# Performance work log

Hardware: AMD Instinct MI355X
Metric: run time of the kernel (lower is better)

Reference implementation:

```python
import jax, jax.numpy as jnp
import numpy as np
from jax import lax

L, B, N, D = 6, 4, 2048, 512
H, DH = 8, 64
ID = H * DH           # 512
M = 266               # int(64*log(64)) random features
INNER = 2 * D         # conformer expansion
K = 31                # depthwise kernel
PAD = (15, 15)        # calc_same_padding(31)
EPS_LN = 1e-5


def setup_inputs() -> dict:
    key = jax.random.key(0)
    ks = jax.random.split(key, 12)
    s = 0.02
    return {
        "x": jax.random.normal(ks[0], (B, N, D), jnp.float32),
        "ln1_g": jnp.ones((L, D), jnp.float32),
        "ln1_b": jnp.zeros((L, D), jnp.float32),
        "wq": jax.random.normal(ks[1], (L, ID, D), jnp.float32) * s,
        "bq": jnp.zeros((L, ID), jnp.float32),
        "wk": jax.random.normal(ks[2], (L, ID, D), jnp.float32) * s,
        "bk": jnp.zeros((L, ID), jnp.float32),
        "wv": jax.random.normal(ks[3], (L, ID, D), jnp.float32) * s,
        "bv": jnp.zeros((L, ID), jnp.float32),
        "wo": jax.random.normal(ks[4], (L, ID, D), jnp.float32) * s,
        "bo": jnp.zeros((L, D), jnp.float32),
        # FAVOR+ random projection buffer (gaussian orthogonal ~ iid gaussian rows)
        "proj": jax.random.normal(ks[5], (L, M, DH), jnp.float32),
        "ln2_g": jnp.ones((L, D), jnp.float32),
        "ln2_b": jnp.zeros((L, D), jnp.float32),
        "pw1_w": jax.random.normal(ks[6], (L, 2 * INNER, D), jnp.float32) * s,
        "pw1_b": jnp.zeros((L, 2 * INNER), jnp.float32),
        "dw_w": jax.random.normal(ks[7], (L, INNER, K), jnp.float32) * s,
        "dw_b": jnp.zeros((L, INNER), jnp.float32),
        "pw2_w": jax.random.normal(ks[8], (L, D, INNER), jnp.float32) * s,
        "pw2_b": jnp.zeros((L, D), jnp.float32),
    }


def layer_norm(x, g, b):
    mu = jnp.mean(x, axis=-1, keepdims=True)
    var = jnp.mean((x - mu) ** 2, axis=-1, keepdims=True)
    return (x - mu) * lax.rsqrt(var + EPS_LN) * g + b


def softmax_kernel(data, proj, is_query, eps=1e-4):
    # data: [b,h,n,dh], proj: [m,dh]
    dn = DH ** -0.25
    ratio = M ** -0.5
    data_dash = jnp.einsum('bhnd,md->bhnm', dn * data, proj)
    diag = jnp.sum(data * data, axis=-1, keepdims=True) * 0.5 * dn * dn  # [b,h,n,1]
    if is_query:
        mx = jnp.max(data_dash, axis=-1, keepdims=True)
        return ratio * (jnp.exp(data_dash - diag - mx) + eps)
    else:
        return ratio * jnp.exp(data_dash - diag + eps)


def favor_attention(q, k, v, proj):
    qp = softmax_kernel(q, proj, True)   # [b,h,n,m]
    kp = softmax_kernel(k, proj, False)  # [b,h,n,m]
    k_cumsum = jnp.sum(kp, axis=-2)      # [b,h,m]
    d_inv = 1.0 / (jnp.einsum('bhnm,bhm->bhn', qp, k_cumsum) + 1e-8)
    context = jnp.einsum('bhnm,bhne->bhme', kp, v)          # [b,h,m,dh]
    out = jnp.einsum('bhme,bhnm,bhn->bhne', context, qp, d_inv)
    return out


def pcmer_forward(x, ln1_g, ln1_b, wq, bq, wk, bk, wv, bv, wo, bo, proj,
                  ln2_g, ln2_b, pw1_w, pw1_b, dw_w, dw_b, pw2_w, pw2_b):
    for l in range(L):
        # --- self attention (FAVOR+) ---
        h = layer_norm(x, ln1_g[l], ln1_b[l])
        q = (h @ wq[l].T + bq[l]).reshape(B, N, H, DH).transpose(0, 2, 1, 3)
        k = (h @ wk[l].T + bk[l]).reshape(B, N, H, DH).transpose(0, 2, 1, 3)
        v = (h @ wv[l].T + bv[l]).reshape(B, N, H, DH).transpose(0, 2, 1, 3)
        o = favor_attention(q, k, v, proj[l])                 # [b,h,n,dh]
        o = o.transpose(0, 2, 1, 3).reshape(B, N, ID)
        x = x + (o @ wo[l].T + bo[l])
        # --- conformer conv module ---
        h = layer_norm(x, ln2_g[l], ln2_b[l])
        y = h @ pw1_w[l].T + pw1_b[l]                         # [b,n,2*inner]
        a, g = y[..., :INNER], y[..., INNER:]
        y = a * jax.nn.sigmoid(g)                             # GLU
        yt = jnp.pad(y.transpose(0, 2, 1), ((0, 0), (0, 0), PAD))  # [b,inner,n+30]
        dw = lax.conv_general_dilated(
            yt, dw_w[l][:, None, :], window_strides=(1,), padding='VALID',
            feature_group_count=INNER,
            dimension_numbers=('NCH', 'OIH', 'NCH')) + dw_b[l][None, :, None]
        dw = jax.nn.silu(dw).transpose(0, 2, 1)               # [b,n,inner]
        x = x + (dw @ pw2_w[l].T + pw2_b[l])
    return x


def reference(x, ln1_g, ln1_b, wq, bq, wk, bk, wv, bv, wo, bo, proj,
              ln2_g, ln2_b, pw1_w, pw1_b, dw_w, dw_b, pw2_w, pw2_b):
    return pcmer_forward(x, ln1_g, ln1_b, wq, bq, wk, bk, wv, bv, wo, bo, proj,
                         ln2_g, ln2_b, pw1_w, pw1_b, dw_w, dw_b, pw2_w, pw2_b)
```

## Files before the change

### kernel.cpp

```cpp
#include <hip/hip_runtime.h>


#define L_LAYERS 6
#define B_ 4
#define N_ 2048
#define D_ 512
#define H_ 8
#define DH_ 64
#define M_ 266
#define INNER_ 1024
#define T_ 8192
#define PS_ 320
#define QKVS_ 1536
#define NS_ 8

typedef __attribute__((ext_vector_type(8))) short short8;
typedef __attribute__((ext_vector_type(4))) float floatx4;

__device__ __forceinline__ ushort f2bf(float f) {
  union { float f; uint u; } v; v.f = f;
  uint r = v.u + 0x7fffu + ((v.u >> 16) & 1u);
  return (ushort)(r >> 16);
}
__device__ __forceinline__ float bf2f(ushort u) {
  union { uint u; float f; } v; v.u = ((uint)u) << 16;
  return v.f;
}
__device__ __forceinline__ float wave_sum(float v) {
#pragma unroll
  for (int m = 1; m < 64; m <<= 1) v += __shfl_xor(v, m);
  return v;
}
__device__ __forceinline__ void async_cp16(const void* g, void* l) {
  __builtin_amdgcn_global_load_lds(
      (const __attribute__((address_space(1))) void*)g,
      (__attribute__((address_space(3))) void*)l, 16, 0, 0);
}

__global__ void f2bf4_kernel(const float4* __restrict__ in, ushort* __restrict__ out, int n4) {
  int i = blockIdx.x * 256 + threadIdx.x;
  if (i < n4) {
    float4 v = in[i];
    ushort4 r;
    r.x = f2bf(v.x); r.y = f2bf(v.y); r.z = f2bf(v.z); r.w = f2bf(v.w);
    *(ushort4*)(out + (size_t)i * 4) = r;
  }
}
__global__ void pack_qkv_w(const float4* __restrict__ src, ushort* __restrict__ dst, int off) {
  int i = blockIdx.x * 256 + threadIdx.x;
  if (i >= L_LAYERS * 512 * 128) return;
  int l = i >> 16;
  int rem = i & 65535;
  int row = rem >> 7, c4 = rem & 127;
  float4 v = src[i];
  ushort4 r;
  r.x = f2bf(v.x); r.y = f2bf(v.y); r.z = f2bf(v.z); r.w = f2bf(v.w);
  *(ushort4*)(dst + ((size_t)l * QKVS_ + off + row) * 512 + c4 * 4) = r;
}
__global__ void pack_qkv_b(const float* __restrict__ bq, const float* __restrict__ bk,
                           const float* __restrict__ bv, float* __restrict__ dst) {
  int i = blockIdx.x * 256 + threadIdx.x;
  if (i >= L_LAYERS * QKVS_) return;
  int l = i / QKVS_, c = i % QKVS_;
  dst[i] = c < 512 ? bq[l * 512 + c] : (c < 1024 ? bk[l * 512 + c - 512] : bv[l * 512 + c - 1024]);
}
__global__ void pad_proj(const float* __restrict__ proj, ushort* __restrict__ dst) {
  int i = blockIdx.x * 256 + threadIdx.x;
  if (i >= L_LAYERS * 320 * 64) return;
  int l = i / (320 * 64), rem = i % (320 * 64), m = rem >> 6, kk = rem & 63;
  dst[i] = (m < M_) ? f2bf(proj[((size_t)l * M_ + m) * 64 + kk]) : (ushort)0;
}
__global__ void pack_pw1_w(const float4* __restrict__ src, ushort* __restrict__ dst) {
  int i = blockIdx.x * 256 + threadIdx.x;
  if (i >= L_LAYERS * 2048 * 128) return;
  int l = i >> 18;
  int rem = i & 262143;
  int cp = rem >> 7, c4 = rem & 127;
  int s = (cp >> 4) & 1;
  int srow = ((cp >> 5) << 4) + (cp & 15) + s * 1024;
  float4 v = src[((size_t)l * 2048 + srow) * 128 + c4];
  ushort4 r;
  r.x = f2bf(v.x); r.y = f2bf(v.y); r.z = f2bf(v.z); r.w = f2bf(v.w);
  *(ushort4*)(dst + ((size_t)l * 2048 + cp) * 512 + c4 * 4) = r;
}
__global__ void pack_pw1_b(const float* __restrict__ src, float* __restrict__ dst) {
  int i = blockIdx.x * 256 + threadIdx.x;
  if (i >= L_LAYERS * 2048) return;
  int l = i >> 11, cp = i & 2047;
  int s = (cp >> 4) & 1;
  int srow = ((cp >> 5) << 4) + (cp & 15) + s * 1024;
  dst[i] = src[l * 2048 + srow];
}

__global__ __launch_bounds__(256) void ln_kernel(const float* __restrict__ x,
                                                 const float* __restrict__ g,
                                                 const float* __restrict__ b,
                                                 ushort* __restrict__ out) {
  const int t = blockIdx.x;
  const int tid = threadIdx.x;
  const float* row = x + (size_t)t * D_;
  float v0 = row[tid], v1 = row[tid + 256];
  float s1 = v0 + v1;
  float s2 = v0 * v0 + v1 * v1;
  s1 = wave_sum(s1);
  s2 = wave_sum(s2);
  __shared__ float sh1[4], sh2[4];
  int w = tid >> 6;
  if ((tid & 63) == 0) { sh1[w] = s1; sh2[w] = s2; }
  __syncthreads();
  s1 = sh1[0] + sh1[1] + sh1[2] + sh1[3];
  s2 = sh2[0] + sh2[1] + sh2[2] + sh2[3];
  float mu = s1 * (1.f / D_);
  float var = s2 * (1.f / D_) - mu * mu;
  float rs = rsqrtf(var + 1e-5f);
  out[(size_t)t * D_ + tid]       = f2bf((v0 - mu) * rs * g[tid] + b[tid]);
  out[(size_t)t * D_ + tid + 256] = f2bf((v1 - mu) * rs * g[tid + 256] + b[tid + 256]);
}

template <bool HAS_RES, bool OUT_BF16, int ACT, int KT>
__global__ __launch_bounds__(256) void gemm_mfma(const ushort* __restrict__ A,
                                                 const ushort* __restrict__ W,
                                                 const float* __restrict__ bias,
                                                 const float* __restrict__ res,
                                                 void* __restrict__ Cout,
                                                 int ldc) {
  constexpr int NT = KT / 32;
  __shared__ ushort As[3][128 * 32];
  __shared__ ushort Bs[3][128 * 32];
  const int tid = threadIdx.x;
  const int w = tid >> 6, lane = tid & 63;
  const int row0 = blockIdx.x * 128, col0 = blockIdx.y * 128;
  const int rl = lane >> 2;
  const int lc = ((lane & 3) ^ ((lane >> 3) & 3)) * 8;
  const ushort* gA0 = A + (size_t)(row0 + w * 32 + rl) * KT + lc;
  const ushort* gA1 = gA0 + (size_t)16 * KT;
  const ushort* gB0 = W + (size_t)(col0 + w * 32 + rl) * KT + lc;
  const ushort* gB1 = gB0 + (size_t)16 * KT;
  const int m16 = lane & 15, quad = lane >> 4;
  const int awr = (w >> 1) * 64, bwc = (w & 1) * 64;
  floatx4 acc[4][4] = {};

  auto stage = [&](int t, int buf) {
    async_cp16(gA0 + t * 32, As[buf] + w * 1024);
    async_cp16(gA1 + t * 32, As[buf] + w * 1024 + 512);
    async_cp16(gB0 + t * 32, Bs[buf] + w * 1024);
    async_cp16(gB1 + t * 32, Bs[buf] + w * 1024 + 512);
  };
  auto body = [&](int buf, bool bar2) {
    short8 af[4], bfr[4];
#pragma unroll
    for (int i = 0; i < 4; i++) {
      int r = awr + i * 16 + m16;
      af[i] = *(const short8*)&As[buf][r * 32 + (quad ^ ((r >> 1) & 3)) * 8];
    }
#pragma unroll
    for (int j = 0; j < 4; j++) {
      int r = bwc + j * 16 + m16;
      bfr[j] = *(const short8*)&Bs[buf][r * 32 + (quad ^ ((r >> 1) & 3)) * 8];
    }
    if (bar2) {
      asm volatile("s_waitcnt lgkmcnt(0)" ::: "memory");
      __builtin_amdgcn_sched_barrier(0);
      __builtin_amdgcn_s_barrier();
    }
#pragma unroll
    for (int i = 0; i < 4; i++)
#pragma unroll
      for (int j = 0; j < 4; j++)
        acc[i][j] = __builtin_amdgcn_mfma_f32_16x16x32_bf16(af[i], bfr[j], acc[i][j], 0, 0, 0);
  };

  stage(0, 0);
  stage(1, 1);
  int c = 0;
  for (int t = 0; t < NT - 2; t++) {
    int pf = c + 2; if (pf >= 3) pf -= 3;
    stage(t + 2, pf);
    asm volatile("s_waitcnt vmcnt(8)" ::: "memory");
    __builtin_amdgcn_s_barrier();
    body(c, true);
    c++; if (c >= 3) c -= 3;
  }
  asm volatile("s_waitcnt vmcnt(4)" ::: "memory");
  __builtin_amdgcn_s_barrier();
  body(c, false);
  c++; if (c >= 3) c -= 3;
  asm volatile("s_waitcnt vmcnt(0)" ::: "memory");
  __builtin_amdgcn_s_barrier();
  body(c, false);

  if (ACT == 0) {
#pragma unroll
    for (int i = 0; i < 4; i++) {
      const int r0 = row0 + awr + i * 16 + quad * 4;
#pragma unroll
      for (int j = 0; j < 4; j++) {
        const int cc = col0 + bwc + j * 16 + m16;
        const float bv = bias[cc];
#pragma unroll
        for (int r = 0; r < 4; r++) {
          float vv = acc[i][j][r] + bv;
          if (HAS_RES) vv += res[(size_t)(r0 + r) * ldc + cc];
          if (OUT_BF16) ((ushort*)Cout)[(size_t)(r0 + r) * ldc + cc] = f2bf(vv);
          else          ((float*)Cout)[(size_t)(r0 + r) * ldc + cc] = vv;
        }
      }
    }
  } else {
#pragma unroll
    for (int i = 0; i < 4; i++) {
      const int r0 = row0 + awr + i * 16 + quad * 4;
#pragma unroll
      for (int jp = 0; jp < 2; jp++) {
        const int j = jp * 2;
        const int ca = col0 + bwc + j * 16 + m16;
        const float ba = bias[ca], bg = bias[ca + 16];
        const int oc = ((col0 + bwc) >> 1) + jp * 16 + m16;
#pragma unroll
        for (int r = 0; r < 4; r++) {
          float a = acc[i][j][r] + ba;
          float g = acc[i][j + 1][r] + bg;
          float z = a / (1.f + expf(-g));
          ((ushort*)Cout)[(size_t)(r0 + r) * ldc + oc] = f2bf(z);
        }
      }
    }
  }
}

__global__ __launch_bounds__(256) void ctx_phi_mfma(const ushort* __restrict__ qkv,
                                                    const ushort* __restrict__ projp,
                                                    float* __restrict__ part,
                                                    float* __restrict__ kpart) {
  __shared__ ushort projs[64 * 64];
  __shared__ ushort kts[32 * 64];
  __shared__ ushort kps[64][40];
  __shared__ ushort vsT[64][40];
  __shared__ float diag_sh[32];
  __shared__ float kshare[4][64];
  const int bh = blockIdx.x, mt = blockIdx.y, ns = blockIdx.z;
  const int b = bh >> 3, h = bh & 7;
  const int m0 = mt * 64;
  const int tid = threadIdx.x;
  const int w = tid >> 6, lane = tid & 63, l16 = lane & 15, quad = lane >> 4;
  const int rl8 = lane >> 3;
  const int lc8 = ((lane & 7) ^ (rl8 & 7)) * 8;
#pragma unroll
  for (int j = 0; j < 2; j++) {
    const int rb = w * 16 + j * 8;
    async_cp16(projp + (size_t)(m0 + rb + rl8) * 64 + lc8, projs + rb * 64);
  }
  const int nn = tid >> 3;
  const int a8 = tid & 7;
  const int gn = nn >> 3, jn = nn & 7;
  const int pc = ((gn ^ (a8 & 3)) << 3) | jn;
  const int km = tid & 63, kg = tid >> 6;
  const float dn = 0.35355339059327373f;
  const float ratio = 0.06131393394849658f;
  floatx4 acc[4] = {};
  float ksp = 0.f;
  for (int nstep = 0; nstep < 2048 / NS_ / 32; nstep++) {
    const int n0 = ns * (2048 / NS_) + nstep * 32;
    {
      const int rb = w * 8;
      async_cp16(qkv + (size_t)(b * N_ + n0 + rb + rl8) * QKVS_ + 512 + h * 64 + lc8,
                 kts + rb * 64);
    }
    uint4 vv = *(const uint4*)(qkv + ((size_t)(b * N_ + n0 + nn)) * QKVS_ + 1024 + h * 64 + a8 * 8);
    __syncthreads();
    {
      const int r = tid >> 3;
      const int c = tid & 7;
      short8 kv8 = *(const short8*)&kts[r * 64 + c * 8];
      const ushort* u = (const ushort*)&kv8;
      float s = 0.f;
#pragma unroll
      for (int j = 0; j < 8; j++) { float f = bf2f(u[j]); s += f * f; }
      s += __shfl_xor(s, 1);
      s += __shfl_xor(s, 2);
      s += __shfl_xor(s, 4);
      if ((tid & 7) == 0) diag_sh[r] = 0.0625f * s;
    }
    {
      const ushort* ve = (const ushort*)&vv;
#pragma unroll
      for (int j = 0; j < 8; j++) vsT[a8 * 8 + j][pc] = ve[j];
    }
    __syncthreads();
    floatx4 pacc[2] = {};
#pragma unroll
    for (int s = 0; s < 2; s++) {
      const int ar = w * 16 + l16;
      short8 af = *(const short8*)&projs[ar * 64 + ((s * 4 + quad) ^ (ar & 7)) * 8];
#pragma unroll
      for (int nj = 0; nj < 2; nj++) {
        const int br = nj * 16 + l16;
        short8 bf = *(const short8*)&kts[br * 64 + ((s * 4 + quad) ^ (br & 7)) * 8];
        pacc[nj] = __builtin_amdgcn_mfma_f32_16x16x32_bf16(af, bf, pacc[nj], 0, 0, 0);
      }
    }
#pragma unroll
    for (int nj = 0; nj < 2; nj++) {
      const int n = nj * 16 + l16;
      const float dgn = diag_sh[n];
#pragma unroll
      for (int r = 0; r < 4; r++) {
        const int m = w * 16 + quad * 4 + r;
        float val = (m0 + m < M_) ? ratio * expf(dn * pacc[nj][r] - dgn + 1e-4f) : 0.f;
        kps[m][(((n >> 3) ^ ((m >> 3) & 3)) << 3) | (n & 7)] = f2bf(val);
      }
    }
    __syncthreads();
    const int am = w * 16 + l16;
    const int apg = quad ^ ((am >> 3) & 3);
    short8 af = *(const short8*)&kps[am][apg * 8];
#pragma unroll
    for (int et = 0; et < 4; et++) {
      const int be = et * 16 + l16;
      const int bpg = quad ^ ((be >> 3) & 3);
      short8 bf = *(const short8*)&vsT[be][bpg * 8];
      acc[et] = __builtin_amdgcn_mfma_f32_16x16x32_bf16(af, bf, acc[et], 0, 0, 0);
    }
    {
      short8 kr = *(const short8*)&kps[km][kg * 8];
      const ushort* ku = (const ushort*)&kr;
#pragma unroll
      for (int j = 0; j < 8; j++) ksp += bf2f(ku[j]);
    }
  }
  float* pb = part + ((size_t)(bh * NS_ + ns) * 5 + mt) * 4096;
#pragma unroll
  for (int et = 0; et < 4; et++)
#pragma unroll
    for (int r = 0; r < 4; r++)
      pb[(w * 16 + quad * 4 + r) * 64 + et * 16 + l16] = acc[et][r];
  kshare[kg][km] = ksp;
  __syncthreads();
  if (tid < 64)
    kpart[((size_t)(bh * NS_ + ns) * 5 + mt) * 64 + tid] =
        kshare[0][tid] + kshare[1][tid] + kshare[2][tid] + kshare[3][tid];
}

__global__ __launch_bounds__(256) void ctx_reduce(const float* __restrict__ part,
                                                  const float* __restrict__ kpart,
                                                  ushort* __restrict__ ctxbT,
                                                  float* __restrict__ ksum) {
  const int bh = blockIdx.x, mt = blockIdx.y;
  const int tid = threadIdx.x;
  const int w = tid >> 6, lane = tid & 63;
  for (int oc = w; oc < 8; oc += 4) {
    const int mbase = mt * 64 + oc * 8;
    if (mbase < 288) {
      float s[8] = {0.f, 0.f, 0.f, 0.f, 0.f, 0.f, 0.f, 0.f};
#pragma unroll
      for (int ns = 0; ns < NS_; ns++) {
        const float* pb = part + ((size_t)(bh * NS_ + ns) * 5 + mt) * 4096;
#pragma unroll
        for (int ml = 0; ml < 8; ml++) s[ml] += pb[(oc * 8 + ml) * 64 + lane];
      }
      ushort tmp[8];
#pragma unroll
      for (int ml = 0; ml < 8; ml++) tmp[ml] = f2bf(s[ml]);
      *(short8*)(ctxbT + ((size_t)(bh * 64 + lane)) * 288 + mbase) = *(const short8*)tmp;
    }
  }
  if (tid < 64) {
    float s = 0.f;
#pragma unroll
    for (int ns = 0; ns < NS_; ns++)
      s += kpart[((size_t)(bh * NS_ + ns) * 5 + mt) * 64 + tid];
    ksum[(size_t)bh * PS_ + mt * 64 + tid] = s;
  }
}

__global__ __launch_bounds__(256, 4) void attn_fused(const ushort* __restrict__ qkv,
                                                     const ushort* __restrict__ projp,
                                                     const ushort* __restrict__ ctxbT,
                                                     const float* __restrict__ ksum,
                                                     ushort* __restrict__ o) {
  __shared__ __align__(16) ushort sm[14336];
  __shared__ float ks_sh[288];
  __shared__ float diag_sh[64];
  ushort* As = sm;
  ushort* Bs = sm + 4096;
  ushort (*qst)[40] = (ushort(*)[40])sm;
  const int bh = blockIdx.x, b = bh >> 3, h = bh & 7;
  const int n0 = blockIdx.y * 64;
  const int tid = threadIdx.x;
  const int w = tid >> 6, lane = tid & 63, l16 = lane & 15, quad = lane >> 4;
  const int rl8 = lane >> 3;
  const int lc8 = ((lane & 7) ^ (rl8 & 7)) * 8;
#pragma unroll
  for (int j = 0; j < 2; j++) {
    const int rb = w * 16 + j * 8;
    async_cp16(qkv + (size_t)(b * N_ + n0 + rb + rl8) * QKVS_ + h * 64 + lc8, As + rb * 64);
  }
#pragma unroll
  for (int j = 0; j < 5; j++) {
    const int rb = w * 40 + j * 8;
    async_cp16(projp + (size_t)(rb + rl8) * 64 + lc8, Bs + rb * 64);
  }
  for (int i = tid; i < 288; i += 256) ks_sh[i] = ksum[(size_t)bh * PS_ + i];
  __syncthreads();
  {
    const int r = w * 16 + (lane >> 2);
    const int c0 = 2 * (lane & 3);
    float s = 0.f;
#pragma unroll
    for (int cc = 0; cc < 2; cc++) {
      short8 vv = *(const short8*)&As[r * 64 + ((c0 + cc) ^ (r & 7)) * 8];
      const ushort* u = (const ushort*)&vv;
#pragma unroll
      for (int j = 0; j < 8; j++) { float f = bf2f(u[j]); s += f * f; }
    }
    s += __shfl_xor(s, 1);
    s += __shfl_xor(s, 2);
    if ((lane & 3) == 0) diag_sh[r] = 0.0625f * s;
  }
  __syncthreads();
  float dgr[4];
#pragma unroll
  for (int r = 0; r < 4; r++) dgr[r] = diag_sh[w * 16 + quad * 4 + r];
  floatx4 acc[18];
#pragma unroll
  for (int cf = 0; cf < 18; cf++) acc[cf] = (floatx4){0.f, 0.f, 0.f, 0.f};
  const int ar = w * 16 + l16;
#pragma unroll
  for (int s = 0; s < 2; s++) {
    short8 af = *(const short8*)&As[ar * 64 + ((s * 4 + quad) ^ (ar & 7)) * 8];
#pragma unroll
    for (int cf = 0; cf < 10; cf++) {
      const int br = cf * 16 + l16;
      short8 bf = *(const short8*)&Bs[br * 64 + ((s * 4 + quad) ^ (br & 7)) * 8];
      acc[cf] = __builtin_amdgcn_mfma_f32_16x16x32_bf16(af, bf, acc[cf], 0, 0, 0);
    }
  }
  __syncthreads();
#pragma unroll
  for (int j = 0; j < 4; j++) {
    const int rb = w * 32 + j * 8;
    async_cp16(projp + (size_t)(160 + rb + rl8) * 64 + lc8, Bs + rb * 64);
  }
  __syncthreads();
#pragma unroll
  for (int s = 0; s < 2; s++) {
    short8 af = *(const short8*)&As[ar * 64 + ((s * 4 + quad) ^ (ar & 7)) * 8];
#pragma unroll
    for (int cf = 10; cf < 18; cf++) {
      const int br = (cf - 10) * 16 + l16;
      short8 bf = *(const short8*)&Bs[br * 64 + ((s * 4 + quad) ^ (br & 7)) * 8];
      acc[cf] = __builtin_amdgcn_mfma_f32_16x16x32_bf16(af, bf, acc[cf], 0, 0, 0);
    }
  }
  const float dn = 0.35355339059327373f;
  const float ratio = 0.06131393394849658f;
  float mxr[4];
#pragma unroll
  for (int r = 0; r < 4; r++) {
    float mx = -1e30f;
#pragma unroll
    for (int cf = 0; cf < 18; cf++) {
      const int col = cf * 16 + l16;
      if (col < M_) mx = fmaxf(mx, dn * acc[cf][r]);
    }
    mx = fmaxf(mx, __shfl_xor(mx, 1));
    mx = fmaxf(mx, __shfl_xor(mx, 2));
    mx = fmaxf(mx, __shfl_xor(mx, 4));
    mx = fmaxf(mx, __shfl_xor(mx, 8));
    mxr[r] = mx;
  }
  __syncthreads();
  float dacc[4] = {0.f, 0.f, 0.f, 0.f};
  floatx4 acc2[4] = {};
  const ushort* ctxrow = ctxbT + (size_t)bh * (64 * 288);
  for (int m0 = 0; m0 < 288; m0 += 32) {
    const int cf0 = m0 >> 4;
#pragma unroll
    for (int cc = 0; cc < 2; cc++) {
      const int col = m0 + cc * 16 + l16;
      const float kv = ks_sh[col];
#pragma unroll
      for (int r = 0; r < 4; r++) {
        float val = (col < M_) ? ratio * (expf(dn * acc[cf0 + cc][r] - dgr[r] - mxr[r]) + 1e-4f)
                               : 0.f;
        qst[w * 16 + quad * 4 + r][cc * 16 + l16] = f2bf(val);
        dacc[r] += val * kv;
      }
    }
    short8 af = *(const short8*)&qst[w * 16 + l16][quad * 8];
#pragma unroll
    for (int et = 0; et < 4; et++) {
      short8 bf = *(const short8*)(ctxrow + (size_t)(et * 16 + l16) * 288 + m0 + quad * 8);
      acc2[et] = __builtin_amdgcn_mfma_f32_16x16x32_bf16(af, bf, acc2[et], 0, 0, 0);
    }
  }
  float di[4];
#pragma unroll
  for (int r = 0; r < 4; r++) {
    float d = dacc[r];
    d += __shfl_xor(d, 1);
    d += __shfl_xor(d, 2);
    d += __shfl_xor(d, 4);
    d += __shfl_xor(d, 8);
    di[r] = 1.f / (d + 1e-8f);
  }
#pragma unroll
  for (int r = 0; r < 4; r++) {
    const int n = n0 + w * 16 + quad * 4 + r;
#pragma unroll
    for (int et = 0; et < 4; et++)
      o[((size_t)(b * N_ + n)) * 512 + h * 64 + et * 16 + l16] = f2bf(acc2[et][r] * di[r]);
  }
}

#define TN_ 16
__global__ __launch_bounds__(256) void dwconv_kernel(const ushort* __restrict__ x,
                                                     const float* __restrict__ w,
                                                     const float* __restrict__ bias,
                                                     ushort* __restrict__ out) {
  const int bid = blockIdx.x;
  const int cb = bid & 3;
  const int nb = (bid >> 2) & 127;
  const int b  = bid >> 9;
  const int c = cb * 256 + threadIdx.x;
  const int n0 = nb * TN_;
  float win[TN_ + 30];
#pragma unroll
  for (int i = 0; i < TN_ + 30; i++) {
    int nn = n0 + i - 15;
    win[i] = (nn >= 0 && nn < N_) ? bf2f(x[(size_t)(b * N_ + nn) * INNER_ + c]) : 0.f;
  }
  float wc[31];
#pragma unroll
  for (int kk = 0; kk < 31; kk++) wc[kk] = w[c * 31 + kk];
  const float bsv = bias[c];
#pragma unroll
  for (int j = 0; j < TN_; j++) {
    float acc = bsv;
#pragma unroll
    for (int kk = 0; kk < 31; kk++) acc += win[j + kk] * wc[kk];
    acc = acc / (1.f + expf(-acc));
    out[(size_t)(b * N_ + n0 + j) * INNER_ + c] = f2bf(acc);
  }
}

extern "C" void kernel_launch(void* const* d_in, const int* in_sizes, int n_in,
                              void* d_out, int out_size, void* d_ws, size_t ws_size,
                              hipStream_t stream) {
  const float* in_x  = (const float*)d_in[0];
  const float* ln1_g = (const float*)d_in[1];
  const float* ln1_b = (const float*)d_in[2];
  const float* wq    = (const float*)d_in[3];
  const float* bq    = (const float*)d_in[4];
  const float* wk    = (const float*)d_in[5];
  const float* bk    = (const float*)d_in[6];
  const float* wv    = (const float*)d_in[7];
  const float* bv    = (const float*)d_in[8];
  const float* wo    = (const float*)d_in[9];
  const float* bo    = (const float*)d_in[10];
  const float* proj  = (const float*)d_in[11];
  const float* ln2_g = (const float*)d_in[12];
  const float* ln2_b = (const float*)d_in[13];
  const float* pw1_w = (const float*)d_in[14];
  const float* pw1_b = (const float*)d_in[15];
  const float* dw_w  = (const float*)d_in[16];
  const float* dw_b  = (const float*)d_in[17];
  const float* pw2_w = (const float*)d_in[18];
  const float* pw2_b = (const float*)d_in[19];

  char* cur = (char*)d_ws;
  auto alloc = [&](size_t bytes) { char* p = cur; cur += (bytes + 255) & ~(size_t)255; return p; };
  float*  x    = (float*)alloc((size_t)T_ * D_ * 4);
  ushort* p    = (ushort*)alloc((size_t)T_ * INNER_ * 2 * 2);
  float*  part = (float*)alloc((size_t)32 * NS_ * 5 * 4096 * 4);
  float*  kpart= (float*)alloc((size_t)32 * NS_ * 5 * 64 * 4);
  ushort* ctxb = (ushort*)alloc((size_t)32 * 288 * 64 * 2);
  float*  ksum = (float*)alloc((size_t)32 * PS_ * 4);
  ushort* h    = (ushort*)alloc((size_t)T_ * D_ * 2);
  ushort* qkv  = (ushort*)alloc((size_t)T_ * QKVS_ * 2);
  ushort* obuf = (ushort*)alloc((size_t)T_ * D_ * 2);
  ushort* wqkv_b = (ushort*)alloc((size_t)L_LAYERS * QKVS_ * 512 * 2);
  float*  bqkv   = (float*)alloc((size_t)L_LAYERS * QKVS_ * 4);
  ushort* wo_b = (ushort*)alloc((size_t)L_LAYERS * D_ * D_ * 2);
  ushort* pjp  = (ushort*)alloc((size_t)L_LAYERS * 320 * 64 * 2);
  ushort* p1_b = (ushort*)alloc((size_t)L_LAYERS * 2048 * D_ * 2);
  float*  pb1  = (float*)alloc((size_t)L_LAYERS * 2048 * 4);
  ushort* p2_b = (ushort*)alloc((size_t)L_LAYERS * D_ * INNER_ * 2);
  ushort* glu  = p;
  ushort* conv = p + (size_t)T_ * INNER_;

  pack_qkv_w<<<(L_LAYERS * 512 * 128 + 255) / 256, 256, 0, stream>>>((const float4*)wq, wqkv_b, 0);
  pack_qkv_w<<<(L_LAYERS * 512 * 128 + 255) / 256, 256, 0, stream>>>((const float4*)wk, wqkv_b, 512);
  pack_qkv_w<<<(L_LAYERS * 512 * 128 + 255) / 256, 256, 0, stream>>>((const float4*)wv, wqkv_b, 1024);
  pack_qkv_b<<<(L_LAYERS * QKVS_ + 255) / 256, 256, 0, stream>>>(bq, bk, bv, bqkv);
  pad_proj<<<(L_LAYERS * 320 * 64 + 255) / 256, 256, 0, stream>>>(proj, pjp);
  pack_pw1_w<<<(L_LAYERS * 2048 * 128 + 255) / 256, 256, 0, stream>>>((const float4*)pw1_w, p1_b);
  pack_pw1_b<<<(L_LAYERS * 2048 + 255) / 256, 256, 0, stream>>>(pw1_b, pb1);
  {
    int n4 = L_LAYERS * D_ * D_ / 4;
    f2bf4_kernel<<<(n4 + 255) / 256, 256, 0, stream>>>((const float4*)wo, wo_b, n4);
    n4 = L_LAYERS * D_ * INNER_ / 4;
    f2bf4_kernel<<<(n4 + 255) / 256, 256, 0, stream>>>((const float4*)pw2_w, p2_b, n4);
  }

  for (int l = 0; l < L_LAYERS; l++) {
    const ushort* wqkvl = wqkv_b + (size_t)l * QKVS_ * 512;
    const ushort* wol = wo_b + (size_t)l * D_ * D_;
    const ushort* pjl = pjp + (size_t)l * 320 * 64;
    const ushort* p1l = p1_b + (size_t)l * 2048 * D_;
    const ushort* p2l = p2_b + (size_t)l * D_ * INNER_;
    const float*  dwl = dw_w + (size_t)l * INNER_ * 31;
    const float*  dwbl = dw_b + (size_t)l * INNER_;
    const float*  xin = (l == 0) ? in_x : x;
    float* xout = (l == L_LAYERS - 1) ? (float*)d_out : x;

    ln_kernel<<<T_, 256, 0, stream>>>(xin, ln1_g + l * D_, ln1_b + l * D_, h);
    gemm_mfma<false, true, 0, 512><<<dim3(T_ / 128, QKVS_ / 128), 256, 0, stream>>>(
        h, wqkvl, bqkv + (size_t)l * QKVS_, nullptr, qkv, QKVS_);
    ctx_phi_mfma<<<dim3(32, 5, NS_), 256, 0, stream>>>(qkv, pjl, part, kpart);
    ctx_reduce<<<dim3(32, 5), 256, 0, stream>>>(part, kpart, ctxb, ksum);
    attn_fused<<<dim3(32, 32), 256, 0, stream>>>(qkv, pjl, ctxb, ksum, obuf);
    gemm_mfma<true, false, 0, 512><<<dim3(T_ / 128, 4), 256, 0, stream>>>(
        obuf, wol, bo + l * D_, xin, x, D_);
    ln_kernel<<<T_, 256, 0, stream>>>(x, ln2_g + l * D_, ln2_b + l * D_, h);
    gemm_mfma<false, true, 1, 512><<<dim3(T_ / 128, 16), 256, 0, stream>>>(
        h, p1l, pb1 + (size_t)l * 2048, nullptr, glu, INNER_);
    dwconv_kernel<<<B_ * (N_ / TN_) * 4, 256, 0, stream>>>(glu, dwl, dwbl, conv);
    gemm_mfma<true, false, 0, 1024><<<dim3(T_ / 128, 4), 256, 0, stream>>>(
        conv, p2l, pw2_b + l * D_, x, xout, D_);
  }
}
```

Before: 1.227 ms.

## Merge weight-packing launches, tune GEMM buffering, and streamline attention and conv kernels

Combines several one-time weight and bias packing kernels into fewer launches. Adds a buffer-count template parameter so the pw1 GEMM uses double instead of triple buffering, which lowers LDS use. In the attention kernel, Q is now loaded straight into registers with a shuffle-based diag reduction, MFMA sections get raised scheduling priority, the max uses a tree reduction, and output goes through LDS for wide coalesced stores. The depthwise conv doubles its tile length, and expf becomes __expf in several places, trading a little accuracy for cheaper math.

```diff
diff --git a/kernel.cpp b/kernel.cpp
--- a/kernel.cpp
+++ b/kernel.cpp
@@ -37,38 +37,55 @@
       (__attribute__((address_space(3))) void*)l, 16, 0, 0);
 }
 
-__global__ void f2bf4_kernel(const float4* __restrict__ in, ushort* __restrict__ out, int n4) {
+__global__ void f2bf4_dual(const float4* __restrict__ s1, int n1,
+                           const float4* __restrict__ s2, int n2,
+                           ushort* __restrict__ out) {
   int i = blockIdx.x * 256 + threadIdx.x;
-  if (i < n4) {
-    float4 v = in[i];
-    ushort4 r;
-    r.x = f2bf(v.x); r.y = f2bf(v.y); r.z = f2bf(v.z); r.w = f2bf(v.w);
-    *(ushort4*)(out + (size_t)i * 4) = r;
-  }
-}
-__global__ void pack_qkv_w(const float4* __restrict__ src, ushort* __restrict__ dst, int off) {
-  int i = blockIdx.x * 256 + threadIdx.x;
-  if (i >= L_LAYERS * 512 * 128) return;
-  int l = i >> 16;
-  int rem = i & 65535;
-  int row = rem >> 7, c4 = rem & 127;
-  float4 v = src[i];
+  if (i >= n1 + n2) return;
+  float4 v = (i < n1) ? s1[i] : s2[i - n1];
   ushort4 r;
   r.x = f2bf(v.x); r.y = f2bf(v.y); r.z = f2bf(v.z); r.w = f2bf(v.w);
-  *(ushort4*)(dst + ((size_t)l * QKVS_ + off + row) * 512 + c4 * 4) = r;
-}
-__global__ void pack_qkv_b(const float* __restrict__ bq, const float* __restrict__ bk,
-                           const float* __restrict__ bv, float* __restrict__ dst) {
+  *(ushort4*)(out + (size_t)i * 4) = r;
+}
+__global__ void pack_qkv_w3(const float4* __restrict__ wq, const float4* __restrict__ wk,
+                            const float4* __restrict__ wv, ushort* __restrict__ dst) {
   int i = blockIdx.x * 256 + threadIdx.x;
-  if (i >= L_LAYERS * QKVS_) return;
-  int l = i / QKVS_, c = i % QKVS_;
-  dst[i] = c < 512 ? bq[l * 512 + c] : (c < 1024 ? bk[l * 512 + c - 512] : bv[l * 512 + c - 1024]);
-}
-__global__ void pad_proj(const float* __restrict__ proj, ushort* __restrict__ dst) {
+  const int per = L_LAYERS * 512 * 128;
+  if (i >= 3 * per) return;
+  int seg = i / per;
+  int rem = i - seg * per;
+  const float4* src = seg == 0 ? wq : (seg == 1 ? wk : wv);
+  int l = rem >> 16;
+  int r2 = rem & 65535;
+  int row = r2 >> 7, c4 = r2 & 127;
+  float4 v = src[rem];
+  ushort4 r;
+  r.x = f2bf(v.x); r.y = f2bf(v.y); r.z = f2bf(v.z); r.w = f2bf(v.w);
+  *(ushort4*)(dst + ((size_t)l * QKVS_ + seg * 512 + row) * 512 + c4 * 4) = r;
+}
+__global__ void pack_small(const float* __restrict__ bq, const float* __restrict__ bk,
+                           const float* __restrict__ bv, float* __restrict__ bqkv,
+                           const float* __restrict__ proj, ushort* __restrict__ pjp,
+                           const float* __restrict__ pw1b, float* __restrict__ pb1) {
   int i = blockIdx.x * 256 + threadIdx.x;
-  if (i >= L_LAYERS * 320 * 64) return;
-  int l = i / (320 * 64), rem = i % (320 * 64), m = rem >> 6, kk = rem & 63;
-  dst[i] = (m < M_) ? f2bf(proj[((size_t)l * M_ + m) * 64 + kk]) : (ushort)0;
+  const int A = L_LAYERS * QKVS_;
+  const int Bn = L_LAYERS * 320 * 64;
+  const int C = L_LAYERS * 2048;
+  if (i < A) {
+    int l = i / QKVS_, c = i % QKVS_;
+    bqkv[i] = c < 512 ? bq[l * 512 + c]
+                      : (c < 1024 ? bk[l * 512 + c - 512] : bv[l * 512 + c - 1024]);
+  } else if (i < A + Bn) {
+    int j = i - A;
+    int l = j / (320 * 64), rem = j % (320 * 64), m = rem >> 6, kk = rem & 63;
+    pjp[j] = (m < M_) ? f2bf(proj[((size_t)l * M_ + m) * 64 + kk]) : (ushort)0;
+  } else if (i < A + Bn + C) {
+    int j = i - A - Bn;
+    int l = j >> 11, cp = j & 2047;
+    int s = (cp >> 4) & 1;
+    int srow = ((cp >> 5) << 4) + (cp & 15) + s * 1024;
+    pb1[j] = pw1b[l * 2048 + srow];
+  }
 }
 __global__ void pack_pw1_w(const float4* __restrict__ src, ushort* __restrict__ dst) {
   int i = blockIdx.x * 256 + threadIdx.x;
@@ -82,14 +99,6 @@
   ushort4 r;
   r.x = f2bf(v.x); r.y = f2bf(v.y); r.z = f2bf(v.z); r.w = f2bf(v.w);
   *(ushort4*)(dst + ((size_t)l * 2048 + cp) * 512 + c4 * 4) = r;
-}
-__global__ void pack_pw1_b(const float* __restrict__ src, float* __restrict__ dst) {
-  int i = blockIdx.x * 256 + threadIdx.x;
-  if (i >= L_LAYERS * 2048) return;
-  int l = i >> 11, cp = i & 2047;
-  int s = (cp >> 4) & 1;
-  int srow = ((cp >> 5) << 4) + (cp & 15) + s * 1024;
-  dst[i] = src[l * 2048 + srow];
 }
 
 __global__ __launch_bounds__(256) void ln_kernel(const float* __restrict__ x,
@@ -117,7 +126,7 @@
   out[(size_t)t * D_ + tid + 256] = f2bf((v1 - mu) * rs * g[tid + 256] + b[tid + 256]);
 }
 
-template <bool HAS_RES, bool OUT_BF16, int ACT, int KT>
+template <bool HAS_RES, bool OUT_BF16, int ACT, int KT, int BUFS>
 __global__ __launch_bounds__(256) void gemm_mfma(const ushort* __restrict__ A,
                                                  const ushort* __restrict__ W,
                                                  const float* __restrict__ bias,
@@ -125,8 +134,8 @@
                                                  void* __restrict__ Cout,
                                                  int ldc) {
   constexpr int NT = KT / 32;
-  __shared__ ushort As[3][128 * 32];
-  __shared__ ushort Bs[3][128 * 32];
+  __shared__ ushort As[BUFS][128 * 32];
+  __shared__ ushort Bs[BUFS][128 * 32];
   const int tid = threadIdx.x;
   const int w = tid >> 6, lane = tid & 63;
   const int row0 = blockIdx.x * 128, col0 = blockIdx.y * 128;
@@ -171,20 +180,23 @@
   };
 
   stage(0, 0);
-  stage(1, 1);
+  if (BUFS == 3) stage(1, 1);
   int c = 0;
-  for (int t = 0; t < NT - 2; t++) {
-    int pf = c + 2; if (pf >= 3) pf -= 3;
-    stage(t + 2, pf);
-    asm volatile("s_waitcnt vmcnt(8)" ::: "memory");
+  for (int t = 0; t < NT - (BUFS - 1); t++) {
+    int pf = c + (BUFS - 1); if (pf >= BUFS) pf -= BUFS;
+    stage(t + BUFS - 1, pf);
+    if (BUFS == 3) { asm volatile("s_waitcnt vmcnt(8)" ::: "memory"); }
+    else           { asm volatile("s_waitcnt vmcnt(4)" ::: "memory"); }
     __builtin_amdgcn_s_barrier();
     body(c, true);
-    c++; if (c >= 3) c -= 3;
-  }
-  asm volatile("s_waitcnt vmcnt(4)" ::: "memory");
-  __builtin_amdgcn_s_barrier();
-  body(c, false);
-  c++; if (c >= 3) c -= 3;
+    c++; if (c >= BUFS) c -= BUFS;
+  }
+  if (BUFS == 3) {
+    asm volatile("s_waitcnt vmcnt(4)" ::: "memory");
+    __builtin_amdgcn_s_barrier();
+    body(c, false);
+    c++; if (c >= BUFS) c -= BUFS;
+  }
   asm volatile("s_waitcnt vmcnt(0)" ::: "memory");
   __builtin_amdgcn_s_barrier();
   body(c, false);
@@ -220,7 +232,7 @@
         for (int r = 0; r < 4; r++) {
           float a = acc[i][j][r] + ba;
           float g = acc[i][j + 1][r] + bg;
-          float z = a / (1.f + expf(-g));
+          float z = a / (1.f + __expf(-g));
           ((ushort*)Cout)[(size_t)(r0 + r) * ldc + oc] = f2bf(z);
         }
       }
@@ -288,6 +300,7 @@
     }
     __syncthreads();
     floatx4 pacc[2] = {};
+    __builtin_amdgcn_s_setprio(1);
 #pragma unroll
     for (int s = 0; s < 2; s++) {
       const int ar = w * 16 + l16;
@@ -299,6 +312,7 @@
         pacc[nj] = __builtin_amdgcn_mfma_f32_16x16x32_bf16(af, bf, pacc[nj], 0, 0, 0);
       }
     }
+    __builtin_amdgcn_s_setprio(0);
 #pragma unroll
     for (int nj = 0; nj < 2; nj++) {
       const int n = nj * 16 + l16;
@@ -306,7 +320,7 @@
 #pragma unroll
       for (int r = 0; r < 4; r++) {
         const int m = w * 16 + quad * 4 + r;
-        float val = (m0 + m < M_) ? ratio * expf(dn * pacc[nj][r] - dgn + 1e-4f) : 0.f;
+        float val = (m0 + m < M_) ? ratio * __expf(dn * pacc[nj][r] - dgn + 1e-4f) : 0.f;
         kps[m][(((n >> 3) ^ ((m >> 3) & 3)) << 3) | (n & 7)] = f2bf(val);
       }
     }
@@ -314,6 +328,7 @@
     const int am = w * 16 + l16;
     const int apg = quad ^ ((am >> 3) & 3);
     short8 af = *(const short8*)&kps[am][apg * 8];
+    __builtin_amdgcn_s_setprio(1);
 #pragma unroll
     for (int et = 0; et < 4; et++) {
       const int be = et * 16 + l16;
@@ -321,6 +336,7 @@
       short8 bf = *(const short8*)&vsT[be][bpg * 8];
       acc[et] = __builtin_amdgcn_mfma_f32_16x16x32_bf16(af, bf, acc[et], 0, 0, 0);
     }
+    __builtin_amdgcn_s_setprio(0);
     {
       short8 kr = *(const short8*)&kps[km][kg * 8];
       const ushort* ku = (const ushort*)&kr;
@@ -378,12 +394,10 @@
                                                      const ushort* __restrict__ ctxbT,
                                                      const float* __restrict__ ksum,
                                                      ushort* __restrict__ o) {
-  __shared__ __align__(16) ushort sm[14336];
+  __shared__ __align__(16) ushort Bs[160 * 64];
+  __shared__ __align__(16) ushort qst[64][40];
+  __shared__ __align__(16) ushort outs[64][64];
   __shared__ float ks_sh[288];
-  __shared__ float diag_sh[64];
-  ushort* As = sm;
-  ushort* Bs = sm + 4096;
-  ushort (*qst)[40] = (ushort(*)[40])sm;
   const int bh = blockIdx.x, b = bh >> 3, h = bh & 7;
   const int n0 = blockIdx.y * 64;
   const int tid = threadIdx.x;
@@ -391,43 +405,38 @@
   const int rl8 = lane >> 3;
   const int lc8 = ((lane & 7) ^ (rl8 & 7)) * 8;
 #pragma unroll
-  for (int j = 0; j < 2; j++) {
-    const int rb = w * 16 + j * 8;
-    async_cp16(qkv + (size_t)(b * N_ + n0 + rb + rl8) * QKVS_ + h * 64 + lc8, As + rb * 64);
-  }
-#pragma unroll
   for (int j = 0; j < 5; j++) {
     const int rb = w * 40 + j * 8;
     async_cp16(projp + (size_t)(rb + rl8) * 64 + lc8, Bs + rb * 64);
   }
   for (int i = tid; i < 288; i += 256) ks_sh[i] = ksum[(size_t)bh * PS_ + i];
+  const ushort* qrow = qkv + (size_t)(b * N_ + n0 + w * 16 + l16) * QKVS_ + h * 64;
+  short8 q0 = *(const short8*)(qrow + quad * 8);
+  short8 q1 = *(const short8*)(qrow + 32 + quad * 8);
+  float dv = 0.f;
+  {
+    const ushort* u0 = (const ushort*)&q0;
+    const ushort* u1 = (const ushort*)&q1;
+#pragma unroll
+    for (int j = 0; j < 8; j++) {
+      float f0 = bf2f(u0[j]), f1 = bf2f(u1[j]);
+      dv += f0 * f0 + f1 * f1;
+    }
+  }
+  dv += __shfl_xor(dv, 16);
+  dv += __shfl_xor(dv, 32);
+  dv *= 0.0625f;
+  float dgr[4];
+#pragma unroll
+  for (int r = 0; r < 4; r++) dgr[r] = __shfl(dv, quad * 4 + r, 16);
   __syncthreads();
-  {
-    const int r = w * 16 + (lane >> 2);
-    const int c0 = 2 * (lane & 3);
-    float s = 0.f;
-#pragma unroll
-    for (int cc = 0; cc < 2; cc++) {
-      short8 vv = *(const short8*)&As[r * 64 + ((c0 + cc) ^ (r & 7)) * 8];
-      const ushort* u = (const ushort*)&vv;
-#pragma unroll
-      for (int j = 0; j < 8; j++) { float f = bf2f(u[j]); s += f * f; }
-    }
-    s += __shfl_xor(s, 1);
-    s += __shfl_xor(s, 2);
-    if ((lane & 3) == 0) diag_sh[r] = 0.0625f * s;
-  }
-  __syncthreads();
-  float dgr[4];
-#pragma unroll
-  for (int r = 0; r < 4; r++) dgr[r] = diag_sh[w * 16 + quad * 4 + r];
   floatx4 acc[18];
 #pragma unroll
   for (int cf = 0; cf < 18; cf++) acc[cf] = (floatx4){0.f, 0.f, 0.f, 0.f};
-  const int ar = w * 16 + l16;
+  __builtin_amdgcn_s_setprio(1);
 #pragma unroll
   for (int s = 0; s < 2; s++) {
-    short8 af = *(const short8*)&As[ar * 64 + ((s * 4 + quad) ^ (ar & 7)) * 8];
+    short8 af = s ? q1 : q0;
 #pragma unroll
     for (int cf = 0; cf < 10; cf++) {
       const int br = cf * 16 + l16;
@@ -435,6 +444,7 @@
       acc[cf] = __builtin_amdgcn_mfma_f32_16x16x32_bf16(af, bf, acc[cf], 0, 0, 0);
     }
   }
+  __builtin_amdgcn_s_setprio(0);
   __syncthreads();
 #pragma unroll
   for (int j = 0; j < 4; j++) {
@@ -442,9 +452,10 @@
     async_cp16(projp + (size_t)(160 + rb + rl8) * 64 + lc8, Bs + rb * 64);
   }
   __syncthreads();
+  __builtin_amdgcn_s_setprio(1);
 #pragma unroll
   for (int s = 0; s < 2; s++) {
-    short8 af = *(const short8*)&As[ar * 64 + ((s * 4 + quad) ^ (ar & 7)) * 8];
+    short8 af = s ? q1 : q0;
 #pragma unroll
     for (int cf = 10; cf < 18; cf++) {
       const int br = (cf - 10) * 16 + l16;
@@ -452,24 +463,29 @@
       acc[cf] = __builtin_amdgcn_mfma_f32_16x16x32_bf16(af, bf, acc[cf], 0, 0, 0);
     }
   }
+  __builtin_amdgcn_s_setprio(0);
   const float dn = 0.35355339059327373f;
   const float ratio = 0.06131393394849658f;
   float mxr[4];
 #pragma unroll
   for (int r = 0; r < 4; r++) {
-    float mx = -1e30f;
+    float v[18];
 #pragma unroll
     for (int cf = 0; cf < 18; cf++) {
       const int col = cf * 16 + l16;
-      if (col < M_) mx = fmaxf(mx, dn * acc[cf][r]);
-    }
+      v[cf] = (col < M_) ? dn * acc[cf][r] : -1e30f;
+    }
+#pragma unroll
+    for (int st = 1; st < 18; st <<= 1)
+#pragma unroll
+      for (int k = 0; k + st < 18; k += 2 * st) v[k] = fmaxf(v[k], v[k + st]);
+    float mx = v[0];
     mx = fmaxf(mx, __shfl_xor(mx, 1));
     mx = fmaxf(mx, __shfl_xor(mx, 2));
     mx = fmaxf(mx, __shfl_xor(mx, 4));
     mx = fmaxf(mx, __shfl_xor(mx, 8));
     mxr[r] = mx;
   }
-  __syncthreads();
   float dacc[4] = {0.f, 0.f, 0.f, 0.f};
   floatx4 acc2[4] = {};
   const ushort* ctxrow = ctxbT + (size_t)bh * (64 * 288);
@@ -481,18 +497,20 @@
       const float kv = ks_sh[col];
 #pragma unroll
       for (int r = 0; r < 4; r++) {
-        float val = (col < M_) ? ratio * (expf(dn * acc[cf0 + cc][r] - dgr[r] - mxr[r]) + 1e-4f)
+        float val = (col < M_) ? ratio * (__expf(dn * acc[cf0 + cc][r] - dgr[r] - mxr[r]) + 1e-4f)
                                : 0.f;
         qst[w * 16 + quad * 4 + r][cc * 16 + l16] = f2bf(val);
         dacc[r] += val * kv;
       }
     }
     short8 af = *(const short8*)&qst[w * 16 + l16][quad * 8];
+    __builtin_amdgcn_s_setprio(1);
 #pragma unroll
     for (int et = 0; et < 4; et++) {
       short8 bf = *(const short8*)(ctxrow + (size_t)(et * 16 + l16) * 288 + m0 + quad * 8);
       acc2[et] = __builtin_amdgcn_mfma_f32_16x16x32_bf16(af, bf, acc2[et], 0, 0, 0);
     }
+    __builtin_amdgcn_s_setprio(0);
   }
   float di[4];
 #pragma unroll
@@ -505,23 +523,27 @@
     di[r] = 1.f / (d + 1e-8f);
   }
 #pragma unroll
-  for (int r = 0; r < 4; r++) {
-    const int n = n0 + w * 16 + quad * 4 + r;
+  for (int r = 0; r < 4; r++)
 #pragma unroll
     for (int et = 0; et < 4; et++)
-      o[((size_t)(b * N_ + n)) * 512 + h * 64 + et * 16 + l16] = f2bf(acc2[et][r] * di[r]);
-  }
-}
-
-#define TN_ 16
+      outs[w * 16 + quad * 4 + r][et * 16 + l16] = f2bf(acc2[et][r] * di[r]);
+#pragma unroll
+  for (int j = 0; j < 2; j++) {
+    const int lr = j * 8 + (lane >> 3);
+    short8 ov = *(const short8*)&outs[w * 16 + lr][(lane & 7) * 8];
+    *(short8*)(o + (size_t)(b * N_ + n0 + w * 16 + lr) * 512 + h * 64 + (lane & 7) * 8) = ov;
+  }
+}
+
+#define TN_ 32
 __global__ __launch_bounds__(256) void dwconv_kernel(const ushort* __restrict__ x,
                                                      const float* __restrict__ w,
                                                      const float* __restrict__ bias,
                                                      ushort* __restrict__ out) {
   const int bid = blockIdx.x;
   const int cb = bid & 3;
-  const int nb = (bid >> 2) & 127;
-  const int b  = bid >> 9;
+  const int nb = (bid >> 2) & (N_ / TN_ - 1);
+  const int b  = bid >> 8;
   const int c = cb * 256 + threadIdx.x;
   const int n0 = nb * TN_;
   float win[TN_ + 30];
@@ -539,7 +561,7 @@
     float acc = bsv;
 #pragma unroll
     for (int kk = 0; kk < 31; kk++) acc += win[j + kk] * wc[kk];
-    acc = acc / (1.f + expf(-acc));
+    acc = acc / (1.f + __expf(-acc));
     out[(size_t)(b * N_ + n0 + j) * INNER_ + c] = f2bf(acc);
   }
 }
@@ -581,26 +603,26 @@
   ushort* obuf = (ushort*)alloc((size_t)T_ * D_ * 2);
   ushort* wqkv_b = (ushort*)alloc((size_t)L_LAYERS * QKVS_ * 512 * 2);
   float*  bqkv   = (float*)alloc((size_t)L_LAYERS * QKVS_ * 4);
-  ushort* wo_b = (ushort*)alloc((size_t)L_LAYERS * D_ * D_ * 2);
+  ushort* wo_b = (ushort*)alloc((size_t)L_LAYERS * D_ * D_ * 2 + (size_t)L_LAYERS * D_ * INNER_ * 2);
+  ushort* p2_b = wo_b + (size_t)L_LAYERS * D_ * D_;
   ushort* pjp  = (ushort*)alloc((size_t)L_LAYERS * 320 * 64 * 2);
   ushort* p1_b = (ushort*)alloc((size_t)L_LAYERS * 2048 * D_ * 2);
   float*  pb1  = (float*)alloc((size_t)L_LAYERS * 2048 * 4);
-  ushort* p2_b = (ushort*)alloc((size_t)L_LAYERS * D_ * INNER_ * 2);
   ushort* glu  = p;
   ushort* conv = p + (size_t)T_ * INNER_;
 
-  pack_qkv_w<<<(L_LAYERS * 512 * 128 + 255) / 256, 256, 0, stream>>>((const float4*)wq, wqkv_b, 0);
-  pack_qkv_w<<<(L_LAYERS * 512 * 128 + 255) / 256, 256, 0, stream>>>((const float4*)wk, wqkv_b, 512);
-  pack_qkv_w<<<(L_LAYERS * 512 * 128 + 255) / 256, 256, 0, stream>>>((const float4*)wv, wqkv_b, 1024);
-  pack_qkv_b<<<(L_LAYERS * QKVS_ + 255) / 256, 256, 0, stream>>>(bq, bk, bv, bqkv);
-  pad_proj<<<(L_LAYERS * 320 * 64 + 255) / 256, 256, 0, stream>>>(proj, pjp);
+  pack_qkv_w3<<<(3 * L_LAYERS * 512 * 128 + 255) / 256, 256, 0, stream>>>(
+      (const float4*)wq, (const float4*)wk, (const float4*)wv, wqkv_b);
   pack_pw1_w<<<(L_LAYERS * 2048 * 128 + 255) / 256, 256, 0, stream>>>((const float4*)pw1_w, p1_b);
-  pack_pw1_b<<<(L_LAYERS * 2048 + 255) / 256, 256, 0, stream>>>(pw1_b, pb1);
   {
-    int n4 = L_LAYERS * D_ * D_ / 4;
-    f2bf4_kernel<<<(n4 + 255) / 256, 256, 0, stream>>>((const float4*)wo, wo_b, n4);
-    n4 = L_LAYERS * D_ * INNER_ / 4;
-    f2bf4_kernel<<<(n4 + 255) / 256, 256, 0, stream>>>((const float4*)pw2_w, p2_b, n4);
+    int n1 = L_LAYERS * D_ * D_ / 4;
+    int n2 = L_LAYERS * D_ * INNER_ / 4;
+    f2bf4_dual<<<(n1 + n2 + 255) / 256, 256, 0, stream>>>(
+        (const float4*)wo, n1, (const float4*)pw2_w, n2, wo_b);
+  }
+  {
+    int tot = L_LAYERS * QKVS_ + L_LAYERS * 320 * 64 + L_LAYERS * 2048;
+    pack_small<<<(tot + 255) / 256, 256, 0, stream>>>(bq, bk, bv, bqkv, proj, pjp, pw1_b, pb1);
   }
 
   for (int l = 0; l < L_LAYERS; l++) {
@@ -615,18 +637,18 @@
     float* xout = (l == L_LAYERS - 1) ? (float*)d_out : x;
 
     ln_kernel<<<T_, 256, 0, stream>>>(xin, ln1_g + l * D_, ln1_b + l * D_, h);
-    gemm_mfma<false, true, 0, 512><<<dim3(T_ / 128, QKVS_ / 128), 256, 0, stream>>>(
+    gemm_mfma<false, true, 0, 512, 3><<<dim3(T_ / 128, QKVS_ / 128), 256, 0, stream>>>(
         h, wqkvl, bqkv + (size_t)l * QKVS_, nullptr, qkv, QKVS_);
     ctx_phi_mfma<<<dim3(32, 5, NS_), 256, 0, stream>>>(qkv, pjl, part, kpart);
     ctx_reduce<<<dim3(32, 5), 256, 0, stream>>>(part, kpart, ctxb, ksum);
     attn_fused<<<dim3(32, 32), 256, 0, stream>>>(qkv, pjl, ctxb, ksum, obuf);
-    gemm_mfma<true, false, 0, 512><<<dim3(T_ / 128, 4), 256, 0, stream>>>(
+    gemm_mfma<true, false, 0, 512, 3><<<dim3(T_ / 128, 4), 256, 0, stream>>>(
         obuf, wol, bo + l * D_, xin, x, D_);
     ln_kernel<<<T_, 256, 0, stream>>>(x, ln2_g + l * D_, ln2_b + l * D_, h);
-    gemm_mfma<false, true, 1, 512><<<dim3(T_ / 128, 16), 256, 0, stream>>>(
+    gemm_mfma<false, true, 1, 512, 2><<<dim3(T_ / 128, 16), 256, 0, stream>>>(
         h, p1l, pb1 + (size_t)l * 2048, nullptr, glu, INNER_);
     dwconv_kernel<<<B_ * (N_ / TN_) * 4, 256, 0, stream>>>(glu, dwl, dwbl, conv);
-    gemm_mfma<true, false, 0, 1024><<<dim3(T_ / 128, 4), 256, 0, stream>>>(
+    gemm_mfma<true, false, 0, 1024, 3><<<dim3(T_ / 128, 4), 256, 0, stream>>>(
         conv, p2l, pw2_b + l * D_, x, xout, D_);
   }
 }
```

New measurement: 1.177 ms. 4.1% less time.
